# Kernel tuning notes

Hardware: AMD Instinct MI355X
Metric: run time of the kernel (lower is better)

## Reference

```python
import jax, jax.numpy as jnp
import numpy as np

B, N, D, H = 4, 2048, 1024, 16
DH = D // H  # head dim = 64


def positional_encoding(n, dim):
    # Faithful vectorization of the numpy double loop in PositionalEncoding.
    i = jnp.arange(dim)
    even_i = (i % 2) == 0
    denom_i = 10000.0 ** (2.0 * jnp.where(even_i, i, i - 1).astype(jnp.float32) / dim)
    pos = jnp.arange(n, dtype=jnp.float32)[:, None]  # [n,1]
    base = jnp.where(even_i[None, :], jnp.sin(pos / denom_i), jnp.cos(pos / denom_i))  # [n,dim]
    p = jnp.arange(n)
    even_p = (p % 2) == 0
    denom_p = 10000.0 ** (2.0 * jnp.where(even_p, p, p - 1).astype(jnp.float32) / n)  # [n]
    j = jnp.arange(dim, dtype=jnp.float32)[None, :]  # [1,dim]
    mult = jnp.where(even_p[:, None], jnp.sin(j / denom_p[:, None]), jnp.cos(j / denom_p[:, None]))  # [n,dim]
    return base * mult


def setup_inputs() -> dict:
    key = jax.random.key(0)
    ks = jax.random.split(key, 4)
    s = 1.0 / np.sqrt(D)
    return {
        "data": jax.random.normal(ks[0], (B, N, D), dtype=jnp.float32),
        "Wq": jax.random.normal(ks[1], (D, D), dtype=jnp.float32) * s,
        "bq": jnp.zeros((D,), dtype=jnp.float32),
        "Wk": jax.random.normal(ks[2], (D, D), dtype=jnp.float32) * s,
        "bk": jnp.zeros((D,), dtype=jnp.float32),
        "Wv": jax.random.normal(ks[3], (D, D), dtype=jnp.float32) * s,
        "bv": jnp.zeros((D,), dtype=jnp.float32),
    }


def _split_heads(x):
    # tf.concat(tf.split(x, H, axis=-1), axis=0): head-major [H*B, N, DH]
    b, n, d = x.shape
    return x.reshape(b, n, H, DH).transpose(2, 0, 1, 3).reshape(H * b, n, DH)


def reference(data, Wq, bq, Wk, bk, Wv, bv):
    b, n, d = data.shape
    x = data + positional_encoding(n, d).astype(data.dtype)  # [B,N,D]
    q = _split_heads(x @ Wq + bq)  # [H*B,N,DH]
    k = _split_heads(x @ Wk + bk)
    v = _split_heads(x @ Wv + bv)
    # scale uses last dim of key AFTER split, i.e. head_dim
    scores = jnp.einsum('bqd,bkd->bqk', q, k) / jnp.sqrt(jnp.float32(DH))  # [H*B,N,N]
    w = jax.nn.softmax(scores, axis=-1)
    return jnp.einsum('bqk,bkd->bqd', w, v)  # [H*B,N,DH]
```

## Files before the change

kernel.cpp:

```cpp
#include <hip/hip_runtime.h>
#include <hip/hip_bf16.h>
#include <hip/hip_fp16.h>

#define BB 4
#define NN 2048
#define DD 1024
#define HH 16
#define DHH 64
#define HB (HH*BB)

typedef __bf16 bf16;
typedef __bf16 bf16x4 __attribute__((ext_vector_type(4)));
typedef __bf16 bf16x8 __attribute__((ext_vector_type(8)));
typedef _Float16 f16x4 __attribute__((ext_vector_type(4)));
typedef float f32x4 __attribute__((ext_vector_type(4)));

#define QSCALE 0.18033688011112042f

__device__ __forceinline__ void async16(const void* g, void* l) {
    __builtin_amdgcn_global_load_lds(
        (const __attribute__((address_space(1))) unsigned int*)g,
        (__attribute__((address_space(3))) unsigned int*)l, 16, 0, 0);
}

__global__ void pe_add_kernel(const float* __restrict__ data, bf16* __restrict__ xb) {
    int t = blockIdx.x * blockDim.x + threadIdx.x;
    int base = t * 4;
    int row = base >> 10;
    int d0 = base & 1023;
    int n = row & (NN - 1);
    const float LOG2_10000 = 13.287712379549449f;
    int pn = n & ~1;
    float denom_p = exp2f((2.0f * (float)pn / (float)NN) * LOG2_10000);
    bool even_p = (n & 1) == 0;
    float4 dv = *(const float4*)(data + base);
    float din[4] = {dv.x, dv.y, dv.z, dv.w};
    bf16x4 ov;
    #pragma unroll
    for (int u = 0; u < 4; ++u) {
        int d = d0 + u;
        int di = d & ~1;
        float denom_i = exp2f((2.0f * (float)di / (float)DD) * LOG2_10000);
        float a = (float)n / denom_i;
        float basev = ((d & 1) == 0) ? __sinf(a) : __cosf(a);
        float bm = (float)d / denom_p;
        float mult = even_p ? __sinf(bm) : __cosf(bm);
        ov[u] = (bf16)(din[u] + basev * mult);
    }
    *(bf16x4*)(xb + base) = ov;
}

__global__ void wtrans_kernel(const float* __restrict__ Wq, const float* __restrict__ Wk,
                              const float* __restrict__ Wv, bf16* __restrict__ Bw) {
    const float* W = (blockIdx.z == 0) ? Wq : (blockIdx.z == 1) ? Wk : Wv;
    bf16* Wt = Bw + (size_t)blockIdx.z * 1024 * 1024;
    __shared__ float s[32][33];
    int bx = blockIdx.x * 32;
    int by = blockIdx.y * 32;
    int tx = threadIdx.x, ty = threadIdx.y;
    #pragma unroll
    for (int i = 0; i < 32; i += 8)
        s[ty + i][tx] = W[(by + ty + i) * DD + bx + tx];
    __syncthreads();
    #pragma unroll
    for (int i = 0; i < 32; i += 8)
        Wt[(size_t)(bx + ty + i) * DD + by + tx] = (bf16)s[tx][ty + i];
}

__launch_bounds__(256)
__global__ void gemm_qkv_fused(const bf16* __restrict__ A,
                               const bf16* __restrict__ Bw,
                               const float* __restrict__ bq, const float* __restrict__ bk,
                               const float* __restrict__ bv,
                               bf16* __restrict__ Qs, bf16* __restrict__ Ks,
                               __half* __restrict__ Vh) {
    __shared__ char smem[32768];
    int tid = threadIdx.x;
    int w = tid >> 6, lane = tid & 63, quad = lane >> 4, l16 = lane & 15;
    int bm = blockIdx.x & 63, bn = blockIdx.x >> 6;
    int m0 = bm * 128, n0 = bn * 128;
    int wm = (w & 1) * 64, wn = (w >> 1) * 64;

    const bf16* aS0 = A + (size_t)(m0 + (tid >> 2)) * DD + (tid & 3) * 8;
    const bf16* aS1 = aS0 + (size_t)64 * DD;
    const bf16* bS0 = Bw + (size_t)(n0 + (tid >> 2)) * DD + (tid & 3) * 8;
    const bf16* bS1 = bS0 + (size_t)64 * DD;

    f32x4 acc[4][4];
    #pragma unroll
    for (int i = 0; i < 4; ++i)
        #pragma unroll
        for (int j = 0; j < 4; ++j) acc[i][j] = (f32x4){0.f, 0.f, 0.f, 0.f};

    async16(aS0, smem + w * 1024);
    async16(aS1, smem + 4096 + w * 1024);
    async16(bS0, smem + 8192 + w * 1024);
    async16(bS1, smem + 12288 + w * 1024);
    __syncthreads();

    for (int kk = 0; kk < DD; kk += 32) {
        char* buf  = smem + ((kk >> 5) & 1) * 16384;
        char* nbuf = smem + (((kk >> 5) & 1) ^ 1) * 16384;
        if (kk + 32 < DD) {
            async16(aS0 + kk + 32, nbuf + w * 1024);
            async16(aS1 + kk + 32, nbuf + 4096 + w * 1024);
            async16(bS0 + kk + 32, nbuf + 8192 + w * 1024);
            async16(bS1 + kk + 32, nbuf + 12288 + w * 1024);
        }
        const bf16* As = (const bf16*)buf;
        const bf16* Bs = (const bf16*)(buf + 8192);
        bf16x8 af[4], bfr[4];
        #pragma unroll
        for (int i = 0; i < 4; ++i)
            af[i] = *(const bf16x8*)(As + (wm + i * 16 + l16) * 32 + quad * 8);
        #pragma unroll
        for (int j = 0; j < 4; ++j)
            bfr[j] = *(const bf16x8*)(Bs + (wn + j * 16 + l16) * 32 + quad * 8);
        #pragma unroll
        for (int i = 0; i < 4; ++i)
            #pragma unroll
            for (int j = 0; j < 4; ++j)
                acc[i][j] = __builtin_amdgcn_mfma_f32_16x16x32_bf16(af[i], bfr[j], acc[i][j], 0, 0, 0);
        __syncthreads();
    }

    int mat = n0 >> 10;
    const float* bias_p = (mat == 0) ? bq : (mat == 1) ? bk : bv;
    #pragma unroll
    for (int j = 0; j < 4; ++j) {
        int ncol = (n0 + wn + j * 16 + l16) & 1023;
        float bias = bias_p[ncol];
        int h = ncol >> 6, dh = ncol & 63;
        #pragma unroll
        for (int i = 0; i < 4; ++i) {
            int mrow0 = m0 + wm + i * 16 + quad * 4;
            int b_ = mrow0 >> 11, nn0 = mrow0 & 2047;
            int hbi = h * BB + b_;
            if (mat == 0) {
                bf16* qp = Qs + ((size_t)hbi * NN + nn0) * DHH + dh;
                #pragma unroll
                for (int r = 0; r < 4; ++r)
                    qp[(size_t)r * DHH] = (bf16)((acc[i][j][r] + bias) * QSCALE);
            } else if (mat == 1) {
                bf16* kp = Ks + ((size_t)hbi * NN + nn0) * DHH + dh;
                #pragma unroll
                for (int r = 0; r < 4; ++r)
                    kp[(size_t)r * DHH] = (bf16)(acc[i][j][r] + bias);
            } else {
                __half* vp = Vh + ((size_t)hbi * DHH + dh) * NN + nn0;
                f16x4 vv;
                #pragma unroll
                for (int r = 0; r < 4; ++r) vv[r] = (_Float16)(acc[i][j][r] + bias);
                *(f16x4*)vp = vv;
            }
        }
    }
}

__launch_bounds__(512)
__global__ void attn_kernel(const bf16* __restrict__ Qs,
                            const bf16* __restrict__ Ks,
                            const __half* __restrict__ Vh,
                            float* __restrict__ out) {
    __shared__ char smem[32768];
    int tid = threadIdx.x;
    int w = tid >> 6, lane = tid & 63, quad = lane >> 4, l16 = lane & 15;
    int bi = blockIdx.x;
    int hb = (bi & 7) | (((bi >> 7) & 7) << 3);
    int q0 = ((bi >> 3) & 15) * 128 + w * 16;

    const bf16* qbase = Qs + ((size_t)hb * NN + q0) * DHH;
    bf16x8 qf0 = *(const bf16x8*)(qbase + (size_t)l16 * DHH + quad * 8);
    bf16x8 qf1 = *(const bf16x8*)(qbase + (size_t)l16 * DHH + quad * 8 + 32);

    int srow = tid >> 3;
    int gch = (tid & 7) ^ (srow & 7);
    const bf16* ksrc = Ks + ((size_t)hb * NN + srow) * DHH + gch * 8;
    const __half* vsrc = Vh + ((size_t)hb * DHH + srow) * NN + gch * 8;

    float m_l = -1e30f;
    f32x4 l_acc = {0.f, 0.f, 0.f, 0.f};
    f32x4 o[4];
    #pragma unroll
    for (int d = 0; d < 4; ++d) o[d] = (f32x4){0.f, 0.f, 0.f, 0.f};
    const f16x4 ones = {(_Float16)1.f, (_Float16)1.f, (_Float16)1.f, (_Float16)1.f};

    int kslot0 = (quad ^ (l16 & 7)) * 8;
    int kslot1 = ((quad ^ 4) ^ (l16 & 7)) * 8;

    async16(ksrc, smem + w * 1024);
    async16(vsrc, smem + 8192 + w * 1024);
    __syncthreads();

    for (int kt = 0; kt < NN; kt += 64) {
        char* buf  = smem + ((kt >> 6) & 1) * 16384;
        char* nbuf = smem + (((kt >> 6) & 1) ^ 1) * 16384;
        if (kt + 64 < NN) {
            async16(ksrc + (size_t)(kt + 64) * DHH, nbuf + w * 1024);
            async16(vsrc + (kt + 64), nbuf + 8192 + w * 1024);
        }
        const bf16* ktile = (const bf16*)buf;
        const char* vtile = buf + 8192;

        f32x4 st[4];
        #pragma unroll
        for (int t = 0; t < 4; ++t) {
            int key = t * 16 + l16;
            bf16x8 kf0 = *(const bf16x8*)(ktile + key * 64 + kslot0);
            bf16x8 kf1 = *(const bf16x8*)(ktile + key * 64 + kslot1);
            f32x4 z = (f32x4){0.f, 0.f, 0.f, 0.f};
            z = __builtin_amdgcn_mfma_f32_16x16x32_bf16(kf0, qf0, z, 0, 0, 0);
            z = __builtin_amdgcn_mfma_f32_16x16x32_bf16(kf1, qf1, z, 0, 0, 0);
            st[t] = z;
        }

        float mx = st[0][0];
        #pragma unroll
        for (int t = 0; t < 4; ++t)
            #pragma unroll
            for (int r = 0; r < 4; ++r) mx = fmaxf(mx, st[t][r]);
        mx = fmaxf(mx, __shfl_xor(mx, 16, 64));
        mx = fmaxf(mx, __shfl_xor(mx, 32, 64));
        float mnew = fmaxf(m_l, mx);
        float alpha = __builtin_amdgcn_exp2f(m_l - mnew);
        m_l = mnew;
        f16x4 p16[4];
        #pragma unroll
        for (int t = 0; t < 4; ++t) {
            #pragma unroll
            for (int r = 0; r < 4; ++r) {
                float p = __builtin_amdgcn_exp2f(st[t][r] - mnew);
                p16[t][r] = (_Float16)p;
            }
        }
        #pragma unroll
        for (int d = 0; d < 4; ++d) o[d] *= alpha;
        l_acc *= alpha;

        #pragma unroll
        for (int d = 0; d < 4; ++d) {
            #pragma unroll
            for (int s = 0; s < 4; ++s) {
                int kc = s * 2 + (quad >> 1);
                int slot = kc ^ (l16 & 7);
                f16x4 vf = *(const f16x4*)(vtile + (d * 16 + l16) * 128 + slot * 16 + (quad & 1) * 8);
                o[d] = __builtin_amdgcn_mfma_f32_16x16x16f16(vf, p16[s], o[d], 0, 0, 0);
            }
        }
        #pragma unroll
        for (int s = 0; s < 4; ++s)
            l_acc = __builtin_amdgcn_mfma_f32_16x16x16f16(ones, p16[s], l_acc, 0, 0, 0);

        __syncthreads();
    }

    float inv = 1.0f / l_acc[0];
    float* ob = out + ((size_t)hb * NN + q0 + l16) * DHH + quad * 4;
    #pragma unroll
    for (int d = 0; d < 4; ++d) {
        f32x4 vv = o[d] * inv;
        *(f32x4*)(ob + d * 16) = vv;
    }
}

extern "C" void kernel_launch(void* const* d_in, const int* in_sizes, int n_in,
                              void* d_out, int out_size, void* d_ws, size_t ws_size,
                              hipStream_t stream) {
    const float* data = (const float*)d_in[0];
    const float* Wq   = (const float*)d_in[1];
    const float* bq   = (const float*)d_in[2];
    const float* Wk   = (const float*)d_in[3];
    const float* bk   = (const float*)d_in[4];
    const float* Wv   = (const float*)d_in[5];
    const float* bv   = (const float*)d_in[6];
    float* out = (float*)d_out;

    char* ws = (char*)d_ws;
    bf16* xb = (bf16*)ws; ws += (size_t)8192 * 1024 * 2;
    bf16* Bw = (bf16*)ws; ws += (size_t)3072 * 1024 * 2;
    bf16* Qs = (bf16*)ws; ws += (size_t)HB * NN * DHH * 2;
    bf16* Ks = (bf16*)ws; ws += (size_t)HB * NN * DHH * 2;
    __half* Vh = (__half*)ws; ws += (size_t)HB * NN * DHH * 2;

    pe_add_kernel<<<8192, 256, 0, stream>>>(data, xb);
    dim3 tb(32, 8), tg(32, 32, 3);
    wtrans_kernel<<<tg, tb, 0, stream>>>(Wq, Wk, Wv, Bw);
    gemm_qkv_fused<<<1536, 256, 0, stream>>>(xb, Bw, bq, bk, bv, Qs, Ks, Vh);
    attn_kernel<<<1024, 512, 0, stream>>>(Qs, Ks, Vh, out);
}
```

Measured before the change: 269.4 us.

## Switch GEMM and attention to 32x32x16 bf16 MFMA with swizzled LDS tiles

Both the QKV projection GEMM and the flash-attention kernel move from 16x16 MFMA tiles to 32x32x16 bf16 MFMA. Attention now uses 256-thread blocks with 32 query rows per wave and keeps V in bf16 instead of fp16. The P fragment is built by exchanging packed bf16 pairs across the half-waves, and the row sum is taken with scalar adds rather than a ones-matrix MFMA. The GEMM gains an XOR-swizzled LDS layout, a block-index remap for locality, and launch bounds for occupancy. The trade-off is more register pressure and scalar rather than vectorized epilogue stores in the GEMM, plus bf16 rounding of P and V in place of fp16.

```diff
diff --git a/kernel.cpp b/kernel.cpp
--- a/kernel.cpp
+++ b/kernel.cpp
@@ -1,6 +1,5 @@
 #include <hip/hip_runtime.h>
 #include <hip/hip_bf16.h>
-#include <hip/hip_fp16.h>
 
 #define BB 4
 #define NN 2048
@@ -10,10 +9,10 @@
 #define HB (HH*BB)
 
 typedef __bf16 bf16;
-typedef __bf16 bf16x4 __attribute__((ext_vector_type(4)));
+typedef __bf16 bf16x4v __attribute__((ext_vector_type(4)));
 typedef __bf16 bf16x8 __attribute__((ext_vector_type(8)));
-typedef _Float16 f16x4 __attribute__((ext_vector_type(4)));
 typedef float f32x4 __attribute__((ext_vector_type(4)));
+typedef float f32x16 __attribute__((ext_vector_type(16)));
 
 #define QSCALE 0.18033688011112042f
 
@@ -21,6 +20,12 @@
     __builtin_amdgcn_global_load_lds(
         (const __attribute__((address_space(1))) unsigned int*)g,
         (__attribute__((address_space(3))) unsigned int*)l, 16, 0, 0);
+}
+
+__device__ __forceinline__ unsigned pkbf(float a, float b) {
+    union { bf16 h[2]; unsigned u; } x;
+    x.h[0] = (bf16)a; x.h[1] = (bf16)b;
+    return x.u;
 }
 
 __global__ void pe_add_kernel(const float* __restrict__ data, bf16* __restrict__ xb) {
@@ -35,7 +40,7 @@
     bool even_p = (n & 1) == 0;
     float4 dv = *(const float4*)(data + base);
     float din[4] = {dv.x, dv.y, dv.z, dv.w};
-    bf16x4 ov;
+    bf16x4v ov;
     #pragma unroll
     for (int u = 0; u < 4; ++u) {
         int d = d0 + u;
@@ -47,7 +52,7 @@
         float mult = even_p ? __sinf(bm) : __cosf(bm);
         ov[u] = (bf16)(din[u] + basev * mult);
     }
-    *(bf16x4*)(xb + base) = ov;
+    *(bf16x4v*)(xb + base) = ov;
 }
 
 __global__ void wtrans_kernel(const float* __restrict__ Wq, const float* __restrict__ Wk,
@@ -67,30 +72,36 @@
         Wt[(size_t)(bx + ty + i) * DD + by + tx] = (bf16)s[tx][ty + i];
 }
 
-__launch_bounds__(256)
+__launch_bounds__(256, 4)
 __global__ void gemm_qkv_fused(const bf16* __restrict__ A,
                                const bf16* __restrict__ Bw,
                                const float* __restrict__ bq, const float* __restrict__ bk,
                                const float* __restrict__ bv,
                                bf16* __restrict__ Qs, bf16* __restrict__ Ks,
-                               __half* __restrict__ Vh) {
+                               bf16* __restrict__ Vb) {
     __shared__ char smem[32768];
     int tid = threadIdx.x;
-    int w = tid >> 6, lane = tid & 63, quad = lane >> 4, l16 = lane & 15;
-    int bm = blockIdx.x & 63, bn = blockIdx.x >> 6;
+    int w = tid >> 6, lane = tid & 63, l32 = lane & 31, hi = lane >> 5;
+    int bi = blockIdx.x;
+    int bn = bi >> 6;
+    int bm = (bi & 7) * 8 + ((bi >> 3) & 7);
     int m0 = bm * 128, n0 = bn * 128;
     int wm = (w & 1) * 64, wn = (w >> 1) * 64;
 
-    const bf16* aS0 = A + (size_t)(m0 + (tid >> 2)) * DD + (tid & 3) * 8;
+    int srow = tid >> 2;
+    int g4 = (tid & 3) ^ (srow & 3);
+    const bf16* aS0 = A + (size_t)(m0 + srow) * DD + g4 * 8;
     const bf16* aS1 = aS0 + (size_t)64 * DD;
-    const bf16* bS0 = Bw + (size_t)(n0 + (tid >> 2)) * DD + (tid & 3) * 8;
+    const bf16* bS0 = Bw + (size_t)(n0 + srow) * DD + g4 * 8;
     const bf16* bS1 = bS0 + (size_t)64 * DD;
 
-    f32x4 acc[4][4];
-    #pragma unroll
-    for (int i = 0; i < 4; ++i)
-        #pragma unroll
-        for (int j = 0; j < 4; ++j) acc[i][j] = (f32x4){0.f, 0.f, 0.f, 0.f};
+    f32x16 acc[2][2];
+    #pragma unroll
+    for (int i = 0; i < 2; ++i)
+        #pragma unroll
+        for (int j = 0; j < 2; ++j)
+            #pragma unroll
+            for (int r = 0; r < 16; ++r) acc[i][j][r] = 0.f;
 
     async16(aS0, smem + w * 1024);
     async16(aS1, smem + 4096 + w * 1024);
@@ -107,159 +118,196 @@
             async16(bS0 + kk + 32, nbuf + 8192 + w * 1024);
             async16(bS1 + kk + 32, nbuf + 12288 + w * 1024);
         }
-        const bf16* As = (const bf16*)buf;
-        const bf16* Bs = (const bf16*)(buf + 8192);
-        bf16x8 af[4], bfr[4];
-        #pragma unroll
-        for (int i = 0; i < 4; ++i)
-            af[i] = *(const bf16x8*)(As + (wm + i * 16 + l16) * 32 + quad * 8);
-        #pragma unroll
-        for (int j = 0; j < 4; ++j)
-            bfr[j] = *(const bf16x8*)(Bs + (wn + j * 16 + l16) * 32 + quad * 8);
-        #pragma unroll
-        for (int i = 0; i < 4; ++i)
-            #pragma unroll
-            for (int j = 0; j < 4; ++j)
-                acc[i][j] = __builtin_amdgcn_mfma_f32_16x16x32_bf16(af[i], bfr[j], acc[i][j], 0, 0, 0);
+        const char* As = buf;
+        const char* Bs = buf + 8192;
+        bf16x8 af[2][2], bfr[2][2];
+        #pragma unroll
+        for (int mt = 0; mt < 2; ++mt) {
+            int row = wm + mt * 32 + l32;
+            #pragma unroll
+            for (int kc = 0; kc < 2; ++kc)
+                af[mt][kc] = *(const bf16x8*)(As + row * 64 + (((kc * 2 + hi)) ^ (l32 & 3)) * 16);
+        }
+        #pragma unroll
+        for (int nt = 0; nt < 2; ++nt) {
+            int row = wn + nt * 32 + l32;
+            #pragma unroll
+            for (int kc = 0; kc < 2; ++kc)
+                bfr[nt][kc] = *(const bf16x8*)(Bs + row * 64 + (((kc * 2 + hi)) ^ (l32 & 3)) * 16);
+        }
+        #pragma unroll
+        for (int mt = 0; mt < 2; ++mt)
+            #pragma unroll
+            for (int nt = 0; nt < 2; ++nt)
+                #pragma unroll
+                for (int kc = 0; kc < 2; ++kc)
+                    acc[mt][nt] = __builtin_amdgcn_mfma_f32_32x32x16_bf16(
+                        af[mt][kc], bfr[nt][kc], acc[mt][nt], 0, 0, 0);
         __syncthreads();
     }
 
     int mat = n0 >> 10;
     const float* bias_p = (mat == 0) ? bq : (mat == 1) ? bk : bv;
     #pragma unroll
-    for (int j = 0; j < 4; ++j) {
-        int ncol = (n0 + wn + j * 16 + l16) & 1023;
+    for (int nt = 0; nt < 2; ++nt) {
+        int ncol = (n0 + wn + nt * 32 + l32) & 1023;
         float bias = bias_p[ncol];
         int h = ncol >> 6, dh = ncol & 63;
         #pragma unroll
-        for (int i = 0; i < 4; ++i) {
-            int mrow0 = m0 + wm + i * 16 + quad * 4;
-            int b_ = mrow0 >> 11, nn0 = mrow0 & 2047;
-            int hbi = h * BB + b_;
-            if (mat == 0) {
-                bf16* qp = Qs + ((size_t)hbi * NN + nn0) * DHH + dh;
+        for (int mt = 0; mt < 2; ++mt) {
+            int rowbase = m0 + wm + mt * 32 + 4 * hi;
+            #pragma unroll
+            for (int m4 = 0; m4 < 4; ++m4) {
                 #pragma unroll
-                for (int r = 0; r < 4; ++r)
-                    qp[(size_t)r * DHH] = (bf16)((acc[i][j][r] + bias) * QSCALE);
-            } else if (mat == 1) {
-                bf16* kp = Ks + ((size_t)hbi * NN + nn0) * DHH + dh;
-                #pragma unroll
-                for (int r = 0; r < 4; ++r)
-                    kp[(size_t)r * DHH] = (bf16)(acc[i][j][r] + bias);
-            } else {
-                __half* vp = Vh + ((size_t)hbi * DHH + dh) * NN + nn0;
-                f16x4 vv;
-                #pragma unroll
-                for (int r = 0; r < 4; ++r) vv[r] = (_Float16)(acc[i][j][r] + bias);
-                *(f16x4*)vp = vv;
+                for (int rr = 0; rr < 4; ++rr) {
+                    int mrow = rowbase + 8 * m4 + rr;
+                    int b_ = mrow >> 11, nn_ = mrow & 2047;
+                    int hbi = h * BB + b_;
+                    float v = acc[mt][nt][m4 * 4 + rr] + bias;
+                    if (mat == 0)
+                        Qs[((size_t)hbi * NN + nn_) * DHH + dh] = (bf16)(v * QSCALE);
+                    else if (mat == 1)
+                        Ks[((size_t)hbi * NN + nn_) * DHH + dh] = (bf16)v;
+                    else
+                        Vb[((size_t)hbi * DHH + dh) * NN + nn_] = (bf16)v;
+                }
             }
         }
     }
 }
 
-__launch_bounds__(512)
+__launch_bounds__(256, 4)
 __global__ void attn_kernel(const bf16* __restrict__ Qs,
                             const bf16* __restrict__ Ks,
-                            const __half* __restrict__ Vh,
+                            const bf16* __restrict__ Vb,
                             float* __restrict__ out) {
     __shared__ char smem[32768];
     int tid = threadIdx.x;
-    int w = tid >> 6, lane = tid & 63, quad = lane >> 4, l16 = lane & 15;
+    int w = tid >> 6, lane = tid & 63, l32 = lane & 31, hi = lane >> 5;
     int bi = blockIdx.x;
-    int hb = (bi & 7) | (((bi >> 7) & 7) << 3);
-    int q0 = ((bi >> 3) & 15) * 128 + w * 16;
-
-    const bf16* qbase = Qs + ((size_t)hb * NN + q0) * DHH;
-    bf16x8 qf0 = *(const bf16x8*)(qbase + (size_t)l16 * DHH + quad * 8);
-    bf16x8 qf1 = *(const bf16x8*)(qbase + (size_t)l16 * DHH + quad * 8 + 32);
+    int xcd = bi & 7, j = bi >> 3;
+    int hb = xcd * 8 + (j & 7);
+    int qb = j >> 3;
+    int q0 = qb * 128 + w * 32;
+
+    const bf16* qbase = Qs + ((size_t)hb * NN + q0 + l32) * DHH + hi * 8;
+    bf16x8 qf[4];
+    #pragma unroll
+    for (int c = 0; c < 4; ++c)
+        qf[c] = *(const bf16x8*)(qbase + c * 16);
 
     int srow = tid >> 3;
-    int gch = (tid & 7) ^ (srow & 7);
-    const bf16* ksrc = Ks + ((size_t)hb * NN + srow) * DHH + gch * 8;
-    const __half* vsrc = Vh + ((size_t)hb * DHH + srow) * NN + gch * 8;
-
-    float m_l = -1e30f;
-    f32x4 l_acc = {0.f, 0.f, 0.f, 0.f};
-    f32x4 o[4];
-    #pragma unroll
-    for (int d = 0; d < 4; ++d) o[d] = (f32x4){0.f, 0.f, 0.f, 0.f};
-    const f16x4 ones = {(_Float16)1.f, (_Float16)1.f, (_Float16)1.f, (_Float16)1.f};
-
-    int kslot0 = (quad ^ (l16 & 7)) * 8;
-    int kslot1 = ((quad ^ 4) ^ (l16 & 7)) * 8;
-
-    async16(ksrc, smem + w * 1024);
-    async16(vsrc, smem + 8192 + w * 1024);
+    int g8 = (tid & 7) ^ (srow & 7);
+    const bf16* ksrc = Ks + ((size_t)hb * NN + srow) * DHH + g8 * 8;
+    const bf16* vsrc = Vb + ((size_t)hb * DHH + srow) * NN + g8 * 8;
+
+    float m_l = -1e30f, lsum = 0.f;
+    f32x16 o[2];
+    #pragma unroll
+    for (int d = 0; d < 2; ++d)
+        #pragma unroll
+        for (int r = 0; r < 16; ++r) o[d][r] = 0.f;
+
+    async16(ksrc,            smem + w * 1024);
+    async16(ksrc + 32 * 64,  smem + 4096 + w * 1024);
+    async16(vsrc,            smem + 8192 + w * 1024);
+    async16(vsrc + 32 * NN,  smem + 12288 + w * 1024);
     __syncthreads();
 
     for (int kt = 0; kt < NN; kt += 64) {
         char* buf  = smem + ((kt >> 6) & 1) * 16384;
         char* nbuf = smem + (((kt >> 6) & 1) ^ 1) * 16384;
         if (kt + 64 < NN) {
-            async16(ksrc + (size_t)(kt + 64) * DHH, nbuf + w * 1024);
-            async16(vsrc + (kt + 64), nbuf + 8192 + w * 1024);
-        }
-        const bf16* ktile = (const bf16*)buf;
+            async16(ksrc + (size_t)(kt + 64) * 64,      nbuf + w * 1024);
+            async16(ksrc + (size_t)(kt + 96) * 64,      nbuf + 4096 + w * 1024);
+            async16(vsrc + (kt + 64),                   nbuf + 8192 + w * 1024);
+            async16(vsrc + (size_t)32 * NN + (kt + 64), nbuf + 12288 + w * 1024);
+        }
+        const char* ktile = buf;
         const char* vtile = buf + 8192;
 
-        f32x4 st[4];
-        #pragma unroll
-        for (int t = 0; t < 4; ++t) {
-            int key = t * 16 + l16;
-            bf16x8 kf0 = *(const bf16x8*)(ktile + key * 64 + kslot0);
-            bf16x8 kf1 = *(const bf16x8*)(ktile + key * 64 + kslot1);
-            f32x4 z = (f32x4){0.f, 0.f, 0.f, 0.f};
-            z = __builtin_amdgcn_mfma_f32_16x16x32_bf16(kf0, qf0, z, 0, 0, 0);
-            z = __builtin_amdgcn_mfma_f32_16x16x32_bf16(kf1, qf1, z, 0, 0, 0);
-            st[t] = z;
-        }
-
-        float mx = st[0][0];
-        #pragma unroll
-        for (int t = 0; t < 4; ++t)
-            #pragma unroll
-            for (int r = 0; r < 4; ++r) mx = fmaxf(mx, st[t][r]);
-        mx = fmaxf(mx, __shfl_xor(mx, 16, 64));
+        f32x16 sa[2];
+        #pragma unroll
+        for (int t = 0; t < 2; ++t) {
+            #pragma unroll
+            for (int r = 0; r < 16; ++r) sa[t][r] = 0.f;
+            int row = t * 32 + l32;
+            #pragma unroll
+            for (int c = 0; c < 4; ++c) {
+                bf16x8 kf = *(const bf16x8*)(ktile + row * 128 + ((c * 2 + hi) ^ (l32 & 7)) * 16);
+                sa[t] = __builtin_amdgcn_mfma_f32_32x32x16_bf16(kf, qf[c], sa[t], 0, 0, 0);
+            }
+        }
+
+        float mx = sa[0][0];
+        #pragma unroll
+        for (int t = 0; t < 2; ++t)
+            #pragma unroll
+            for (int r = 0; r < 16; ++r) mx = fmaxf(mx, sa[t][r]);
         mx = fmaxf(mx, __shfl_xor(mx, 32, 64));
         float mnew = fmaxf(m_l, mx);
         float alpha = __builtin_amdgcn_exp2f(m_l - mnew);
         m_l = mnew;
-        f16x4 p16[4];
-        #pragma unroll
-        for (int t = 0; t < 4; ++t) {
-            #pragma unroll
-            for (int r = 0; r < 4; ++r) {
-                float p = __builtin_amdgcn_exp2f(st[t][r] - mnew);
-                p16[t][r] = (_Float16)p;
+
+        float ts = 0.f;
+        unsigned dw[2][4][2];
+        #pragma unroll
+        for (int t = 0; t < 2; ++t) {
+            #pragma unroll
+            for (int m4 = 0; m4 < 4; ++m4) {
+                float p0 = __builtin_amdgcn_exp2f(sa[t][m4 * 4 + 0] - mnew);
+                float p1 = __builtin_amdgcn_exp2f(sa[t][m4 * 4 + 1] - mnew);
+                float p2 = __builtin_amdgcn_exp2f(sa[t][m4 * 4 + 2] - mnew);
+                float p3 = __builtin_amdgcn_exp2f(sa[t][m4 * 4 + 3] - mnew);
+                ts += (p0 + p1) + (p2 + p3);
+                dw[t][m4][0] = pkbf(p0, p1);
+                dw[t][m4][1] = pkbf(p2, p3);
             }
         }
-        #pragma unroll
-        for (int d = 0; d < 4; ++d) o[d] *= alpha;
-        l_acc *= alpha;
-
-        #pragma unroll
-        for (int d = 0; d < 4; ++d) {
-            #pragma unroll
-            for (int s = 0; s < 4; ++s) {
-                int kc = s * 2 + (quad >> 1);
-                int slot = kc ^ (l16 & 7);
-                f16x4 vf = *(const f16x4*)(vtile + (d * 16 + l16) * 128 + slot * 16 + (quad & 1) * 8);
-                o[d] = __builtin_amdgcn_mfma_f32_16x16x16f16(vf, p16[s], o[d], 0, 0, 0);
+        ts += __shfl_xor(ts, 32, 64);
+        lsum = lsum * alpha + ts;
+        #pragma unroll
+        for (int d = 0; d < 2; ++d)
+            #pragma unroll
+            for (int r = 0; r < 16; ++r) o[d][r] *= alpha;
+
+        #pragma unroll
+        for (int c = 0; c < 4; ++c) {
+            int t = c >> 1, mlo = (c & 1) * 2;
+            unsigned a0 = dw[t][mlo][0],     a1 = dw[t][mlo][1];
+            unsigned b0 = dw[t][mlo + 1][0], b1 = dw[t][mlo + 1][1];
+            unsigned own0 = hi ? b0 : a0, own1 = hi ? b1 : a1;
+            unsigned snd0 = hi ? a0 : b0, snd1 = hi ? a1 : b1;
+            unsigned rcv0 = __shfl_xor(snd0, 32, 64);
+            unsigned rcv1 = __shfl_xor(snd1, 32, 64);
+            union { unsigned u[4]; bf16x8 v; } pu;
+            pu.u[0] = hi ? rcv0 : own0;
+            pu.u[1] = hi ? rcv1 : own1;
+            pu.u[2] = hi ? own0 : rcv0;
+            pu.u[3] = hi ? own1 : rcv1;
+            #pragma unroll
+            for (int d = 0; d < 2; ++d) {
+                int row = d * 32 + l32;
+                bf16x8 vf = *(const bf16x8*)(vtile + row * 128 + ((c * 2 + hi) ^ (l32 & 7)) * 16);
+                o[d] = __builtin_amdgcn_mfma_f32_32x32x16_bf16(vf, pu.v, o[d], 0, 0, 0);
             }
         }
-        #pragma unroll
-        for (int s = 0; s < 4; ++s)
-            l_acc = __builtin_amdgcn_mfma_f32_16x16x16f16(ones, p16[s], l_acc, 0, 0, 0);
-
         __syncthreads();
     }
 
-    float inv = 1.0f / l_acc[0];
-    float* ob = out + ((size_t)hb * NN + q0 + l16) * DHH + quad * 4;
-    #pragma unroll
-    for (int d = 0; d < 4; ++d) {
-        f32x4 vv = o[d] * inv;
-        *(f32x4*)(ob + d * 16) = vv;
+    float inv = 1.0f / lsum;
+    float* ob = out + ((size_t)hb * NN + q0 + l32) * DHH + 4 * hi;
+    #pragma unroll
+    for (int d = 0; d < 2; ++d) {
+        #pragma unroll
+        for (int m4 = 0; m4 < 4; ++m4) {
+            f32x4 vv;
+            vv[0] = o[d][m4 * 4 + 0] * inv;
+            vv[1] = o[d][m4 * 4 + 1] * inv;
+            vv[2] = o[d][m4 * 4 + 2] * inv;
+            vv[3] = o[d][m4 * 4 + 3] * inv;
+            *(f32x4*)(ob + d * 32 + 8 * m4) = vv;
+        }
     }
 }
 
@@ -280,11 +328,11 @@
     bf16* Bw = (bf16*)ws; ws += (size_t)3072 * 1024 * 2;
     bf16* Qs = (bf16*)ws; ws += (size_t)HB * NN * DHH * 2;
     bf16* Ks = (bf16*)ws; ws += (size_t)HB * NN * DHH * 2;
-    __half* Vh = (__half*)ws; ws += (size_t)HB * NN * DHH * 2;
+    bf16* Vb = (bf16*)ws; ws += (size_t)HB * NN * DHH * 2;
 
     pe_add_kernel<<<8192, 256, 0, stream>>>(data, xb);
     dim3 tb(32, 8), tg(32, 32, 3);
     wtrans_kernel<<<tg, tb, 0, stream>>>(Wq, Wk, Wv, Bw);
-    gemm_qkv_fused<<<1536, 256, 0, stream>>>(xb, Bw, bq, bk, bv, Qs, Ks, Vh);
-    attn_kernel<<<1024, 512, 0, stream>>>(Qs, Ks, Vh, out);
-}
+    gemm_qkv_fused<<<1536, 256, 0, stream>>>(xb, Bw, bq, bk, bv, Qs, Ks, Vb);
+    attn_kernel<<<1024, 256, 0, stream>>>(Qs, Ks, Vb, out);
+}
```

Measured after the change: 292.1 us. 1.08x slower.
